# Kernel optimization log

Hardware: AMD Instinct MI355X
Metric: run time of the kernel (lower is better)

The kernel has to match this reference:

```python
import jax, jax.numpy as jnp
import numpy as np

N_NODES, N_EDGES, D = 50000, 1250000, 64
N_LAYERS = 3


def setup_inputs() -> dict:
    key = jax.random.key(0)
    ks = jax.random.split(key, 6)
    sc = 1.0 / np.sqrt(D)  # ~xavier scale for 64->64 linears
    return {
        "in_feat": jax.random.normal(ks[0], (N_NODES, D), jnp.float32),
        "src": jax.random.randint(ks[1], (N_EDGES,), 0, N_NODES, dtype=jnp.int32),
        "dst": jax.random.randint(ks[2], (N_EDGES,), 0, N_NODES, dtype=jnp.int32),
        "W_pool": jax.random.normal(ks[3], (N_LAYERS, D, D), jnp.float32) * sc,
        "b_pool": jnp.zeros((N_LAYERS, D), jnp.float32),
        "W_self": jax.random.normal(ks[4], (N_LAYERS, D, D), jnp.float32) * sc,
        "W_neigh": jax.random.normal(ks[5], (N_LAYERS, D, D), jnp.float32) * sc,
        "bias": jnp.zeros((N_LAYERS, D), jnp.float32),
    }


def reference(in_feat, src, dst, W_pool, b_pool, W_self, W_neigh, bias):
    # Dropout is identity in eval mode and omitted for determinism.
    n = in_feat.shape[0]
    h = in_feat
    for l in range(N_LAYERS):
        # per-edge pool MLP: relu(W_pool h_src + b_pool)  -> [E, D]
        m = jax.nn.relu(h[src] @ W_pool[l] + b_pool[l])
        # max-pool aggregation over incoming edges of each dst node
        agg = jax.ops.segment_max(m, dst, num_segments=n)
        # nodes with no in-edges get -inf from segment_max -> DGL uses 0
        agg = jnp.where(jnp.isfinite(agg), agg, 0.0)
        h = h @ W_self[l] + agg @ W_neigh[l] + bias[l]
        if l < N_LAYERS - 1:
            h = jax.nn.relu(h)
    return h
```

## Files before the change

### kernel.cpp

```cpp
#include <hip/hip_runtime.h>


#define NN 50000
#define NE 1250000
#define DD 64

#define BSH 7
#define NB1 391
#define CHUNK 2048
#define NBLK1 611

#define GEMM_BLOCKS 782
#define CAST_BLOCKS 400
#define NMAT 9

using bf16x8 = __attribute__((ext_vector_type(8))) short;
using f32x4  = __attribute__((ext_vector_type(4))) float;

__device__ __forceinline__ f32x4 mfma16(bf16x8 a, bf16x8 b, f32x4 c) {
    return __builtin_amdgcn_mfma_f32_16x16x32_bf16(a, b, c, 0, 0, 0);
}

__device__ __forceinline__ unsigned int f32_to_bf16_bits(float f) {
    unsigned int u = __float_as_uint(f);
    return (u + 0x7FFFu + ((u >> 16) & 1u)) >> 16;
}
__device__ __forceinline__ unsigned int pack2bf16(float a, float b) {
    return f32_to_bf16_bits(a) | (f32_to_bf16_bits(b) << 16);
}


__global__ __launch_bounds__(256) void fat1(const int* __restrict__ dst,
                                            int* __restrict__ H,
                                            const float* __restrict__ in_feat,
                                            unsigned short* __restrict__ h0,
                                            const float* __restrict__ Wp,
                                            const float* __restrict__ Ws,
                                            const float* __restrict__ Wn,
                                            unsigned short* __restrict__ wb) {
    __shared__ int hist[NB1];
    int tid = threadIdx.x;
    int bx = blockIdx.x;
    if (bx < NBLK1) {
        for (int i = tid; i < NB1; i += 256) hist[i] = 0;
        __syncthreads();
        int base = bx * CHUNK;
        int end = min(base + CHUNK, NE);
        for (int i = base + tid; i < end; i += 256) atomicAdd(&hist[dst[i] >> BSH], 1);
        __syncthreads();
        for (int k = tid; k < NB1; k += 256) H[k * NBLK1 + bx] = hist[k];
        return;
    }
    if (bx < NBLK1 + CAST_BLOCKS) {
        const float4* inv = (const float4*)in_feat;
        uint4* ov = (uint4*)h0;
        int t = (bx - NBLK1) * 256 + tid;
        for (int u = t; u < (NN * DD) / 8; u += CAST_BLOCKS * 256) {
            float4 f0 = inv[u * 2], f1 = inv[u * 2 + 1];
            uint4 o;
            o.x = pack2bf16(f0.x, f0.y);
            o.y = pack2bf16(f0.z, f0.w);
            o.z = pack2bf16(f1.x, f1.y);
            o.w = pack2bf16(f1.z, f1.w);
            ov[u] = o;
        }
        return;
    }
    int m = bx - NBLK1 - CAST_BLOCKS;
    const float* srcW = (m < 3) ? (Wp + (size_t)m * DD * DD)
                    : (m < 6) ? (Ws + (size_t)(m - 3) * DD * DD)
                              : (Wn + (size_t)(m - 6) * DD * DD);
    unsigned short* dstW = wb + (size_t)m * 512 * 8;
    for (int idx = tid; idx < 512; idx += 256) {
        int lane = idx & 63, cc = (idx >> 6) & 3, s = idx >> 8;
        int col = cc * 16 + (lane & 15);
        int kb = s * 32 + ((lane >> 4) << 3);
#pragma unroll
        for (int j = 0; j < 8; ++j)
            dstW[idx * 8 + j] = (unsigned short)f32_to_bf16_bits(srcW[(kb + j) * DD + col]);
    }
}


__device__ __forceinline__ void load_A(const unsigned short* __restrict__ h,
                                       int row0, int lane, bf16x8& a0, bf16x8& a1) {
    int r = row0 + (lane & 15);
    int kk = (lane >> 4) * 8;
    a0 = bf16x8{0, 0, 0, 0, 0, 0, 0, 0};
    a1 = a0;
    if (r < NN) {
        a0 = *(const bf16x8*)(h + (size_t)r * DD + kk);
        a1 = *(const bf16x8*)(h + (size_t)r * DD + kk + 32);
    }
}


__global__ __launch_bounds__(256) void fat2(const int* __restrict__ H,
                                            int* __restrict__ rowsum,
                                            int* __restrict__ colbase,
                                            int* __restrict__ ticket,
                                            const unsigned short* __restrict__ h0,
                                            const unsigned short* __restrict__ wb,
                                            const float* __restrict__ bp,
                                            unsigned short* __restrict__ z) {
    __shared__ int s[256];
    __shared__ int isLast;
    int tid = threadIdx.x;
    int bx = blockIdx.x;
    if (bx < NB1) {
        int k = bx;
        int v = 0;
        for (int b = tid; b < NBLK1; b += 256) v += H[k * NBLK1 + b];
        s[tid] = v;
        __syncthreads();
        for (int o = 128; o > 0; o >>= 1) {
            if (tid < o) s[tid] += s[tid + o];
            __syncthreads();
        }
        if (tid == 0) {
            atomicExch(&rowsum[k], s[0]);
            __threadfence();
            isLast = (atomicAdd(ticket, 1) == NB1 - 1);
        }
        __syncthreads();
        if (!isLast) return;
        if (tid < 64) {
            int running = 0;
            for (int b0 = 0; b0 < NB1; b0 += 64) {
                int idx = b0 + tid;
                int val = (idx < NB1) ? atomicAdd(&rowsum[idx], 0) : 0;
                int incl = val;
#pragma unroll
                for (int o = 1; o < 64; o <<= 1) {
                    int up = __shfl_up(incl, o);
                    if (tid >= o) incl += up;
                }
                if (idx < NB1) colbase[idx] = running + (incl - val);
                running += __shfl(incl, 63);
            }
            if (tid == 0) colbase[NB1] = running;
        }
        return;
    }
    int lane = tid & 63;
    int row0 = (bx - NB1) * 64 + (tid >> 6) * 16;
    bf16x8 a0, a1;
    load_A(h0, row0, lane, a0, a1);
    const bf16x8* WB = (const bf16x8*)wb;
    f32x4 acc[4];
#pragma unroll
    for (int c = 0; c < 4; ++c) {
        float bv = bp[c * 16 + (lane & 15)];
        acc[c] = f32x4{bv, bv, bv, bv};
        acc[c] = mfma16(a0, WB[(0 * 4 + c) * 64 + lane], acc[c]);
        acc[c] = mfma16(a1, WB[(1 * 4 + c) * 64 + lane], acc[c]);
    }
    int rbase = row0 + (lane >> 4) * 4;
#pragma unroll
    for (int reg = 0; reg < 4; ++reg) {
        int row = rbase + reg;
        if (row < NN) {
#pragma unroll
            for (int c = 0; c < 4; ++c)
                z[(size_t)row * DD + c * 16 + (lane & 15)] =
                    (unsigned short)f32_to_bf16_bits(fmaxf(acc[c][reg], 0.f));
        }
    }
}


__global__ __launch_bounds__(256) void k3_offsets(int* __restrict__ H,
                                                  const int* __restrict__ colbase) {
    int wid = (blockIdx.x * blockDim.x + threadIdx.x) >> 6;
    int lane = threadIdx.x & 63;
    if (wid >= NB1) return;
    int running = colbase[wid];
    int* row = H + wid * NBLK1;
    for (int b0 = 0; b0 < NBLK1; b0 += 64) {
        int idx = b0 + lane;
        int v = (idx < NBLK1) ? row[idx] : 0;
        int incl = v;
#pragma unroll
        for (int o = 1; o < 64; o <<= 1) {
            int up = __shfl_up(incl, o);
            if (lane >= o) incl += up;
        }
        if (idx < NBLK1) row[idx] = running + (incl - v);
        running += __shfl(incl, 63);
    }
}

__global__ __launch_bounds__(256) void p1_scatter(const int* __restrict__ dst,
                                                  const int* __restrict__ src,
                                                  const int* __restrict__ H,
                                                  int* __restrict__ pairs, int e) {
    __shared__ int off[NB1];
    __shared__ int cursor[NB1];
    int tid = threadIdx.x;
    for (int i = tid; i < NB1; i += 256) {
        off[i] = H[i * NBLK1 + blockIdx.x];
        cursor[i] = 0;
    }
    __syncthreads();
    int base = blockIdx.x * CHUNK;
    int end = min(base + CHUNK, e);
    for (int i = base + tid; i < end; i += 256) {
        int d = dst[i];
        int k = d >> BSH;
        int pos = off[k] + atomicAdd(&cursor[k], 1);
        pairs[pos] = ((d & 127) << 16) | src[i];
    }
}

__global__ __launch_bounds__(256) void p2_bucket(const int* __restrict__ pairs,
                                                 const int* __restrict__ colbase,
                                                 int* __restrict__ rowptr,
                                                 unsigned short* __restrict__ edge_src) {
    __shared__ int cnt[128];
    __shared__ int curi[128];
    __shared__ int sbuf[2][128];
    int k = blockIdx.x;
    int tid = threadIdx.x;
    int beg = colbase[k], end = colbase[k + 1];
    if (tid < 128) { cnt[tid] = 0; curi[tid] = 0; }
    __syncthreads();
    for (int i = beg + tid; i < end; i += 256) atomicAdd(&cnt[pairs[i] >> 16], 1);
    __syncthreads();
    if (tid < 128) sbuf[0][tid] = cnt[tid];
    __syncthreads();
    int cur = 0;
    for (int o = 1; o < 128; o <<= 1) {
        if (tid < 128) sbuf[cur ^ 1][tid] = sbuf[cur][tid] + ((tid >= o) ? sbuf[cur][tid - o] : 0);
        cur ^= 1;
        __syncthreads();
    }
    int node0 = k << BSH;
    if (tid < 128) {
        int excl = sbuf[cur][tid] - cnt[tid];
        curi[tid] = beg + excl;
        int node = node0 + tid;
        if (node < NN) rowptr[node] = beg + excl;
    }
    __syncthreads();
    for (int i = beg + tid; i < end; i += 256) {
        int p = pairs[i];
        int pos = atomicAdd(&curi[p >> 16], 1);
        edge_src[pos] = (unsigned short)(p & 0xFFFF);
    }
    if (k == 0 && tid == 0) rowptr[NN] = NE;
}


__global__ __launch_bounds__(256) void gemm_fused_mfma(const unsigned short* __restrict__ h,
                                                       const unsigned short* __restrict__ agg,
                                                       const unsigned short* __restrict__ wbs,
                                                       const unsigned short* __restrict__ wbn,
                                                       const unsigned short* __restrict__ wbp,
                                                       const float* __restrict__ b,
                                                       const float* __restrict__ bp,
                                                       unsigned short* __restrict__ hn_out,
                                                       unsigned short* __restrict__ z) {
    __shared__ unsigned short hnl[4][16 * 72];
    int tid = threadIdx.x;
    int w = tid >> 6, lane = tid & 63;
    int row0 = blockIdx.x * 64 + w * 16;
    bf16x8 ah0, ah1, ag0, ag1;
    load_A(h, row0, lane, ah0, ah1);
    load_A(agg, row0, lane, ag0, ag1);
    const bf16x8* WS = (const bf16x8*)wbs;
    const bf16x8* WN = (const bf16x8*)wbn;
    const bf16x8* WP = (const bf16x8*)wbp;
    f32x4 acc[4];
#pragma unroll
    for (int c = 0; c < 4; ++c) {
        float bv = b[c * 16 + (lane & 15)];
        acc[c] = f32x4{bv, bv, bv, bv};
        acc[c] = mfma16(ah0, WS[(0 * 4 + c) * 64 + lane], acc[c]);
        acc[c] = mfma16(ah1, WS[(1 * 4 + c) * 64 + lane], acc[c]);
        acc[c] = mfma16(ag0, WN[(0 * 4 + c) * 64 + lane], acc[c]);
        acc[c] = mfma16(ag1, WN[(1 * 4 + c) * 64 + lane], acc[c]);
    }
    int rloc = (lane >> 4) * 4;
    int rbase = row0 + rloc;
#pragma unroll
    for (int reg = 0; reg < 4; ++reg) {
        int row = rbase + reg;
#pragma unroll
        for (int c = 0; c < 4; ++c) {
            unsigned short us =
                (unsigned short)f32_to_bf16_bits(fmaxf(acc[c][reg], 0.f));
            hnl[w][(rloc + reg) * 72 + c * 16 + (lane & 15)] = us;
            if (row < NN) hn_out[(size_t)row * DD + c * 16 + (lane & 15)] = us;
        }
    }
    int kk = (lane >> 4) * 8;
    bf16x8 p0 = *(const bf16x8*)&hnl[w][(lane & 15) * 72 + kk];
    bf16x8 p1 = *(const bf16x8*)&hnl[w][(lane & 15) * 72 + kk + 32];
    f32x4 acc2[4];
#pragma unroll
    for (int c = 0; c < 4; ++c) {
        float bv = bp[c * 16 + (lane & 15)];
        acc2[c] = f32x4{bv, bv, bv, bv};
        acc2[c] = mfma16(p0, WP[(0 * 4 + c) * 64 + lane], acc2[c]);
        acc2[c] = mfma16(p1, WP[(1 * 4 + c) * 64 + lane], acc2[c]);
    }
#pragma unroll
    for (int reg = 0; reg < 4; ++reg) {
        int row = rbase + reg;
        if (row < NN) {
#pragma unroll
            for (int c = 0; c < 4; ++c)
                z[(size_t)row * DD + c * 16 + (lane & 15)] =
                    (unsigned short)f32_to_bf16_bits(fmaxf(acc2[c][reg], 0.f));
        }
    }
}

__global__ __launch_bounds__(256) void gemm_final_mfma(const unsigned short* __restrict__ h,
                                                       const unsigned short* __restrict__ agg,
                                                       const unsigned short* __restrict__ wbs,
                                                       const unsigned short* __restrict__ wbn,
                                                       const float* __restrict__ b,
                                                       float* __restrict__ out) {
    int tid = threadIdx.x;
    int lane = tid & 63;
    int row0 = blockIdx.x * 64 + (tid >> 6) * 16;
    bf16x8 ah0, ah1, ag0, ag1;
    load_A(h, row0, lane, ah0, ah1);
    load_A(agg, row0, lane, ag0, ag1);
    const bf16x8* WS = (const bf16x8*)wbs;
    const bf16x8* WN = (const bf16x8*)wbn;
    f32x4 acc[4];
#pragma unroll
    for (int c = 0; c < 4; ++c) {
        float bv = b[c * 16 + (lane & 15)];
        acc[c] = f32x4{bv, bv, bv, bv};
        acc[c] = mfma16(ah0, WS[(0 * 4 + c) * 64 + lane], acc[c]);
        acc[c] = mfma16(ah1, WS[(1 * 4 + c) * 64 + lane], acc[c]);
        acc[c] = mfma16(ag0, WN[(0 * 4 + c) * 64 + lane], acc[c]);
        acc[c] = mfma16(ag1, WN[(1 * 4 + c) * 64 + lane], acc[c]);
    }
    int rbase = row0 + (lane >> 4) * 4;
#pragma unroll
    for (int reg = 0; reg < 4; ++reg) {
        int row = rbase + reg;
        if (row < NN) {
#pragma unroll
            for (int c = 0; c < 4; ++c)
                out[(size_t)row * DD + c * 16 + (lane & 15)] = acc[c][reg];
        }
    }
}


__device__ __forceinline__ unsigned int pkmax(unsigned int a, unsigned int b) {
    unsigned int r;
    asm("v_pk_max_u16 %0, %1, %2" : "=v"(r) : "v"(a), "v"(b));
    return r;
}

__global__ __launch_bounds__(256) void agg_max(const unsigned short* __restrict__ z,
                                               const int* __restrict__ rowptr,
                                               const unsigned short* __restrict__ edge_src,
                                               unsigned short* __restrict__ agg, int n) {
    int wslot = __builtin_amdgcn_readfirstlane((int)((blockIdx.x * blockDim.x + threadIdx.x) >> 6));
    int nslots = (gridDim.x * blockDim.x) >> 6;
    int lane = threadIdx.x & 63;
    int eg = lane >> 3;
    int fo = (lane & 7) * 8;
    for (int node = wslot; node < n; node += nslots) {
        int beg = rowptr[node];
        int end = rowptr[node + 1];
        unsigned int m0 = 0, m1 = 0, m2 = 0, m3 = 0;
        int e = beg;
#pragma unroll 2
        for (; e + 8 <= end; e += 8) {
            int s = edge_src[e + eg];
            uint4 a = *(const uint4*)(z + (size_t)s * DD + fo);
            m0 = pkmax(m0, a.x);
            m1 = pkmax(m1, a.y);
            m2 = pkmax(m2, a.z);
            m3 = pkmax(m3, a.w);
        }
        if (e + eg < end) {
            int s = edge_src[e + eg];
            uint4 a = *(const uint4*)(z + (size_t)s * DD + fo);
            m0 = pkmax(m0, a.x);
            m1 = pkmax(m1, a.y);
            m2 = pkmax(m2, a.z);
            m3 = pkmax(m3, a.w);
        }
#pragma unroll
        for (int o = 8; o < 64; o <<= 1) {
            m0 = pkmax(m0, (unsigned int)__shfl_xor((int)m0, o));
            m1 = pkmax(m1, (unsigned int)__shfl_xor((int)m1, o));
            m2 = pkmax(m2, (unsigned int)__shfl_xor((int)m2, o));
            m3 = pkmax(m3, (unsigned int)__shfl_xor((int)m3, o));
        }
        if (eg == 0) {
            uint4 o;
            o.x = m0; o.y = m1; o.z = m2; o.w = m3;
            *(uint4*)(agg + (size_t)node * DD + fo) = o;
        }
    }
}


extern "C" void kernel_launch(void* const* d_in, const int* in_sizes, int n_in,
                              void* d_out, int out_size, void* d_ws, size_t ws_size,
                              hipStream_t stream) {
    const float* in_feat = (const float*)d_in[0];
    const int* src = (const int*)d_in[1];
    const int* dst = (const int*)d_in[2];
    const float* W_pool = (const float*)d_in[3];
    const float* b_pool = (const float*)d_in[4];
    const float* W_self = (const float*)d_in[5];
    const float* W_neigh = (const float*)d_in[6];
    const float* bias = (const float*)d_in[7];
    float* out = (float*)d_out;

    char* ws = (char*)d_ws;
    size_t off = 0;
    auto alloc = [&](size_t bytes) -> void* {
        void* p = (void*)(ws + off);
        off += (bytes + 255) & ~(size_t)255;
        return p;
    };
    int* rowptr              = (int*)alloc((NN + 1) * sizeof(int));
    int* H                   = (int*)alloc((size_t)NB1 * NBLK1 * sizeof(int));
    int* rowsum              = (int*)alloc(NB1 * sizeof(int));
    int* colbase             = (int*)alloc((NB1 + 1) * sizeof(int));
    int* ticket              = (int*)alloc(sizeof(int));
    unsigned short* edge_src = (unsigned short*)alloc((size_t)NE * sizeof(unsigned short));
    unsigned short* z        = (unsigned short*)alloc((size_t)NN * DD * sizeof(unsigned short));
    unsigned short* agg      = (unsigned short*)alloc((size_t)NN * DD * sizeof(unsigned short));
    unsigned short* h0       = (unsigned short*)alloc((size_t)NN * DD * sizeof(unsigned short));
    unsigned short* h1       = (unsigned short*)alloc((size_t)NN * DD * sizeof(unsigned short));
    unsigned short* h2       = (unsigned short*)alloc((size_t)NN * DD * sizeof(unsigned short));
    unsigned short* wb       = (unsigned short*)alloc((size_t)NMAT * 512 * 8 * sizeof(unsigned short));
    int* pairs               = (int*)alloc((size_t)NE * sizeof(int));
    (void)ws_size; (void)in_sizes; (void)n_in; (void)out_size;

    hipMemsetAsync(ticket, 0, sizeof(int), stream);

    auto WBp = [&](int l) { return wb + (size_t)(0 + l) * 4096; };
    auto WBs = [&](int l) { return wb + (size_t)(3 + l) * 4096; };
    auto WBn = [&](int l) { return wb + (size_t)(6 + l) * 4096; };

    fat1<<<NBLK1 + CAST_BLOCKS + NMAT, 256, 0, stream>>>(
        dst, H, in_feat, h0, W_pool, W_self, W_neigh, wb);
    fat2<<<NB1 + GEMM_BLOCKS, 256, 0, stream>>>(
        H, rowsum, colbase, ticket, h0, wb, b_pool, z);
    k3_offsets<<<(NB1 * 64 + 255) / 256, 256, 0, stream>>>(H, colbase);
    p1_scatter<<<NBLK1, 256, 0, stream>>>(dst, src, H, pairs, NE);
    p2_bucket<<<NB1, 256, 0, stream>>>(pairs, colbase, rowptr, edge_src);

    agg_max<<<2048, 256, 0, stream>>>(z, rowptr, edge_src, agg, NN);
    gemm_fused_mfma<<<GEMM_BLOCKS, 256, 0, stream>>>(
        h0, agg, WBs(0), WBn(0), WBp(1), bias, b_pool + DD, h1, z);
    agg_max<<<2048, 256, 0, stream>>>(z, rowptr, edge_src, agg, NN);
    gemm_fused_mfma<<<GEMM_BLOCKS, 256, 0, stream>>>(
        h1, agg, WBs(1), WBn(1), WBp(2), bias + DD, b_pool + 2 * DD, h2, z);
    agg_max<<<2048, 256, 0, stream>>>(z, rowptr, edge_src, agg, NN);
    gemm_final_mfma<<<GEMM_BLOCKS, 256, 0, stream>>>(
        h2, agg, WBs(2), WBn(2), bias + 2 * DD, out);
}
```

Baseline: 173.2 us.

## Stage edge bucketing through shared memory and widen buckets to 256 nodes

The CSR-building scatter kernels now do a local counting sort in LDS before writing to global memory. Pairs, and later edge sources, are written out in contiguous runs instead of being scattered one at a time. Buckets grow from 128 to 256 destination nodes and each scatter block handles 8192 edges, which cuts the number of blocks and histogram columns. The cost is extra shared memory, more barriers, and a binary search per element to find each bucket's global offset; p2 falls back to direct scatter when a bucket has more than 16384 edges.

```diff
diff --git a/kernel.cpp b/kernel.cpp
--- a/kernel.cpp
+++ b/kernel.cpp
@@ -5,10 +5,10 @@
 #define NE 1250000
 #define DD 64
 
-#define BSH 7
-#define NB1 391
-#define CHUNK 2048
-#define NBLK1 611
+#define BSH 8
+#define NB1 196
+#define CHUNK 8192
+#define NBLK1 153
 
 #define GEMM_BLOCKS 782
 #define CAST_BLOCKS 400
@@ -195,20 +195,49 @@
                                                   const int* __restrict__ H,
                                                   int* __restrict__ pairs, int e) {
     __shared__ int off[NB1];
+    __shared__ int lbase[NB1 + 1];
     __shared__ int cursor[NB1];
-    int tid = threadIdx.x;
+    __shared__ int sbuf[2][256];
+    __shared__ int sorted[CHUNK];
+    int tid = threadIdx.x, bx = blockIdx.x;
     for (int i = tid; i < NB1; i += 256) {
-        off[i] = H[i * NBLK1 + blockIdx.x];
+        off[i] = H[i * NBLK1 + bx];
         cursor[i] = 0;
     }
-    __syncthreads();
-    int base = blockIdx.x * CHUNK;
+    if (tid < 256) sbuf[0][tid] = 0;
+    __syncthreads();
+    int base = bx * CHUNK;
     int end = min(base + CHUNK, e);
+    int L = end - base;
+    for (int i = base + tid; i < end; i += 256) atomicAdd(&sbuf[0][dst[i] >> BSH], 1);
+    __syncthreads();
+    int myCnt = sbuf[0][tid];
+    __syncthreads();
+    sbuf[0][tid] = myCnt;
+    __syncthreads();
+    int cur = 0;
+    for (int o = 1; o < 256; o <<= 1) {
+        sbuf[cur ^ 1][tid] = sbuf[cur][tid] + ((tid >= o) ? sbuf[cur][tid - o] : 0);
+        cur ^= 1;
+        __syncthreads();
+    }
+    if (tid < NB1) lbase[tid] = sbuf[cur][tid] - myCnt;
+    if (tid == 0) lbase[NB1] = L;
+    __syncthreads();
     for (int i = base + tid; i < end; i += 256) {
         int d = dst[i];
         int k = d >> BSH;
-        int pos = off[k] + atomicAdd(&cursor[k], 1);
-        pairs[pos] = ((d & 127) << 16) | src[i];
+        int r = atomicAdd(&cursor[k], 1);
+        sorted[lbase[k] + r] = ((d & 255) << 16) | src[i];
+    }
+    __syncthreads();
+    for (int t = tid; t < L; t += 256) {
+        int lo = 0, hi = NB1;
+        while (hi - lo > 1) {
+            int mid = (lo + hi) >> 1;
+            if (t >= lbase[mid]) lo = mid; else hi = mid;
+        }
+        pairs[off[lo] + (t - lbase[lo])] = sorted[t];
     }
 }
 
@@ -216,36 +245,47 @@
                                                  const int* __restrict__ colbase,
                                                  int* __restrict__ rowptr,
                                                  unsigned short* __restrict__ edge_src) {
-    __shared__ int cnt[128];
-    __shared__ int curi[128];
-    __shared__ int sbuf[2][128];
+    __shared__ int cnt[256];
+    __shared__ int base2[256];
+    __shared__ int cur2[256];
+    __shared__ int sbuf[2][256];
+    __shared__ unsigned short stage[16384];
     int k = blockIdx.x;
     int tid = threadIdx.x;
     int beg = colbase[k], end = colbase[k + 1];
-    if (tid < 128) { cnt[tid] = 0; curi[tid] = 0; }
+    int len = end - beg;
+    cnt[tid] = 0;
+    cur2[tid] = 0;
     __syncthreads();
     for (int i = beg + tid; i < end; i += 256) atomicAdd(&cnt[pairs[i] >> 16], 1);
     __syncthreads();
-    if (tid < 128) sbuf[0][tid] = cnt[tid];
+    sbuf[0][tid] = cnt[tid];
     __syncthreads();
     int cur = 0;
-    for (int o = 1; o < 128; o <<= 1) {
-        if (tid < 128) sbuf[cur ^ 1][tid] = sbuf[cur][tid] + ((tid >= o) ? sbuf[cur][tid - o] : 0);
+    for (int o = 1; o < 256; o <<= 1) {
+        sbuf[cur ^ 1][tid] = sbuf[cur][tid] + ((tid >= o) ? sbuf[cur][tid - o] : 0);
         cur ^= 1;
         __syncthreads();
     }
-    int node0 = k << BSH;
-    if (tid < 128) {
-        int excl = sbuf[cur][tid] - cnt[tid];
-        curi[tid] = beg + excl;
-        int node = node0 + tid;
-        if (node < NN) rowptr[node] = beg + excl;
-    }
-    __syncthreads();
-    for (int i = beg + tid; i < end; i += 256) {
-        int p = pairs[i];
-        int pos = atomicAdd(&curi[p >> 16], 1);
-        edge_src[pos] = (unsigned short)(p & 0xFFFF);
+    int excl = sbuf[cur][tid] - cnt[tid];
+    base2[tid] = excl;
+    int node = (k << BSH) + tid;
+    if (node < NN) rowptr[node] = beg + excl;
+    __syncthreads();
+    if (len <= 16384) {
+        for (int i = beg + tid; i < end; i += 256) {
+            int p = pairs[i];
+            int r = atomicAdd(&cur2[p >> 16], 1);
+            stage[base2[p >> 16] + r] = (unsigned short)(p & 0xFFFF);
+        }
+        __syncthreads();
+        for (int t = tid; t < len; t += 256) edge_src[beg + t] = stage[t];
+    } else {
+        for (int i = beg + tid; i < end; i += 256) {
+            int p = pairs[i];
+            int r = atomicAdd(&cur2[p >> 16], 1);
+            edge_src[beg + base2[p >> 16] + r] = (unsigned short)(p & 0xFFFF);
+        }
     }
     if (k == 0 && tid == 0) rowptr[NN] = NE;
 }
```

New measurement: 186.7 us. 7.8% more time.
